# Kernel tuning notes

Hardware: AMD Instinct MI355X
Metric: run time of the kernel (lower is better)

Reference implementation:

```python
import jax, jax.numpy as jnp
import numpy as np


def setup_inputs() -> dict:
    key = jax.random.key(0)
    x = jax.random.normal(key, (32, 4096, 128), dtype=jnp.float32)
    return {"x": x, "window_size": 5}


def reference(x, window_size):
    # Circular pad along dim=1 by (w-1) using the leading slice, as in the torch code.
    w = window_size
    dim = 1
    if w > 1:
        pad = jax.lax.slice_in_dim(x, 0, w - 1, axis=dim)
        xp = jnp.concatenate([x, pad], axis=dim)  # [B, L+w-1, C]
    else:
        xp = x
    L = x.shape[dim]
    # Sliding windows of size w along dim=1: stack w shifted views -> [B, L, C, w]
    windows = jnp.stack(
        [jax.lax.slice_in_dim(xp, i, i + L, axis=dim) for i in range(w)], axis=-1
    )
    # torch.median returns the lower median: sorted[(w-1)//2]
    med = jnp.sort(windows, axis=-1)[..., (w - 1) // 2]  # [B, L, C]
    return med
```

## Files before the change

kernel.cpp:

```cpp
#include <hip/hip_runtime.h>


constexpr int B   = 32;
constexpr int L   = 4096;
constexpr int C   = 128;
constexpr int C4  = C / 4;
constexpr int RPT = 4;
constexpr int LG  = L / RPT;

typedef float f32x4 __attribute__((ext_vector_type(4)));

__device__ __forceinline__ f32x4 f4min(f32x4 a, f32x4 b) {
    f32x4 r;
    r.x = fminf(a.x, b.x); r.y = fminf(a.y, b.y);
    r.z = fminf(a.z, b.z); r.w = fminf(a.w, b.w);
    return r;
}
__device__ __forceinline__ f32x4 f4max(f32x4 a, f32x4 b) {
    f32x4 r;
    r.x = fmaxf(a.x, b.x); r.y = fmaxf(a.y, b.y);
    r.z = fmaxf(a.z, b.z); r.w = fmaxf(a.w, b.w);
    return r;
}

#define SORT2(x, y) { f32x4 _lo = f4min(x, y); f32x4 _hi = f4max(x, y); (x) = _lo; (y) = _hi; }

__device__ __forceinline__ f32x4 median5(f32x4 v0, f32x4 v1, f32x4 v2,
                                         f32x4 v3, f32x4 v4) {
    SORT2(v0, v1);
    SORT2(v3, v4);
    SORT2(v2, v4);
    SORT2(v2, v3);
    SORT2(v1, v4);
    SORT2(v0, v3);
    SORT2(v0, v2);
    SORT2(v1, v3);
    SORT2(v1, v2);
    return v2;
}

__global__ __launch_bounds__(256)
void MedianPool_73426760893099_kernel(const f32x4* __restrict__ x,
                                      f32x4* __restrict__ out) {
    const int idx = blockIdx.x * blockDim.x + threadIdx.x;
    const int c4 = idx & (C4 - 1);
    const int lg = (idx >> 5) & (LG - 1);
    const int b  = idx >> 15;

    const f32x4* __restrict__ xb = x + (size_t)b * L * C4;
    const int l0 = lg * RPT;

    f32x4 r0 = xb[(size_t)((l0 + 0) & (L - 1)) * C4 + c4];
    f32x4 r1 = xb[(size_t)((l0 + 1) & (L - 1)) * C4 + c4];
    f32x4 r2 = xb[(size_t)((l0 + 2) & (L - 1)) * C4 + c4];
    f32x4 r3 = xb[(size_t)((l0 + 3) & (L - 1)) * C4 + c4];
    f32x4 r4 = xb[(size_t)((l0 + 4) & (L - 1)) * C4 + c4];
    f32x4 r5 = xb[(size_t)((l0 + 5) & (L - 1)) * C4 + c4];
    f32x4 r6 = xb[(size_t)((l0 + 6) & (L - 1)) * C4 + c4];
    f32x4 r7 = xb[(size_t)((l0 + 7) & (L - 1)) * C4 + c4];

    f32x4 m0 = median5(r0, r1, r2, r3, r4);
    f32x4 m1 = median5(r1, r2, r3, r4, r5);
    f32x4 m2 = median5(r2, r3, r4, r5, r6);
    f32x4 m3 = median5(r3, r4, r5, r6, r7);

    f32x4* o = out + (size_t)b * L * C4 + (size_t)l0 * C4 + c4;
    __builtin_nontemporal_store(m0, o + 0 * C4);
    __builtin_nontemporal_store(m1, o + 1 * C4);
    __builtin_nontemporal_store(m2, o + 2 * C4);
    __builtin_nontemporal_store(m3, o + 3 * C4);
}

extern "C" void kernel_launch(void* const* d_in, const int* in_sizes, int n_in,
                              void* d_out, int out_size, void* d_ws, size_t ws_size,
                              hipStream_t stream) {
    const f32x4* x   = (const f32x4*)d_in[0];
    f32x4*       out = (f32x4*)d_out;

    const int threads = B * LG * C4;
    const int block   = 256;
    const int grid    = threads / block;
    MedianPool_73426760893099_kernel<<<grid, block, 0, stream>>>(x, out);
}
```

Measured before the change: 26.11 us.

## Use med3 median-of-5 network, 8 rows per thread, and XCD block swizzle

Replaces the 9-compare-exchange median-of-5 network with a shorter min/max sequence that ends in the hardware fmed3 instruction. Each thread now produces 8 output rows instead of 4, so the halo overhead drops from 8 loads per 4 outputs to 12 loads per 8 outputs. Block IDs are remapped so that contiguous work lands on the same XCD, which is meant to improve L2 reuse of the overlapping halo rows. The cost is more registers per thread and half as many threads in flight.

```diff
diff --git a/kernel.cpp b/kernel.cpp
--- a/kernel.cpp
+++ b/kernel.cpp
@@ -5,8 +5,9 @@
 constexpr int L   = 4096;
 constexpr int C   = 128;
 constexpr int C4  = C / 4;
-constexpr int RPT = 4;
+constexpr int RPT = 8;
 constexpr int LG  = L / RPT;
+constexpr int NXCD = 8;
 
 typedef float f32x4 __attribute__((ext_vector_type(4)));
 
@@ -22,53 +23,51 @@
     r.z = fmaxf(a.z, b.z); r.w = fmaxf(a.w, b.w);
     return r;
 }
+__device__ __forceinline__ f32x4 f4med3(f32x4 a, f32x4 b, f32x4 c) {
+    f32x4 r;
+    r.x = __builtin_amdgcn_fmed3f(a.x, b.x, c.x);
+    r.y = __builtin_amdgcn_fmed3f(a.y, b.y, c.y);
+    r.z = __builtin_amdgcn_fmed3f(a.z, b.z, c.z);
+    r.w = __builtin_amdgcn_fmed3f(a.w, b.w, c.w);
+    return r;
+}
 
-#define SORT2(x, y) { f32x4 _lo = f4min(x, y); f32x4 _hi = f4max(x, y); (x) = _lo; (y) = _hi; }
-
-__device__ __forceinline__ f32x4 median5(f32x4 v0, f32x4 v1, f32x4 v2,
-                                         f32x4 v3, f32x4 v4) {
-    SORT2(v0, v1);
-    SORT2(v3, v4);
-    SORT2(v2, v4);
-    SORT2(v2, v3);
-    SORT2(v1, v4);
-    SORT2(v0, v3);
-    SORT2(v0, v2);
-    SORT2(v1, v3);
-    SORT2(v1, v2);
-    return v2;
+__device__ __forceinline__ f32x4 median5(f32x4 a, f32x4 b, f32x4 c,
+                                         f32x4 d, f32x4 e) {
+    f32x4 t1 = f4min(a, b), t2 = f4max(a, b);
+    f32x4 t3 = f4min(c, d), t4 = f4max(c, d);
+    f32x4 t5 = f4max(t1, t3);
+    f32x4 t6 = f4min(t2, t4);
+    return f4med3(t5, t6, e);
 }
 
 __global__ __launch_bounds__(256)
 void MedianPool_73426760893099_kernel(const f32x4* __restrict__ x,
                                       f32x4* __restrict__ out) {
-    const int idx = blockIdx.x * blockDim.x + threadIdx.x;
+    const int nwg  = gridDim.x;
+    const int cpx  = nwg / NXCD;
+    const int bid  = (int)blockIdx.x;
+    const int bsw  = (bid % NXCD) * cpx + bid / NXCD;
+
+    const int idx = bsw * blockDim.x + threadIdx.x;
     const int c4 = idx & (C4 - 1);
     const int lg = (idx >> 5) & (LG - 1);
-    const int b  = idx >> 15;
+    const int b  = idx >> 14;
 
     const f32x4* __restrict__ xb = x + (size_t)b * L * C4;
     const int l0 = lg * RPT;
 
-    f32x4 r0 = xb[(size_t)((l0 + 0) & (L - 1)) * C4 + c4];
-    f32x4 r1 = xb[(size_t)((l0 + 1) & (L - 1)) * C4 + c4];
-    f32x4 r2 = xb[(size_t)((l0 + 2) & (L - 1)) * C4 + c4];
-    f32x4 r3 = xb[(size_t)((l0 + 3) & (L - 1)) * C4 + c4];
-    f32x4 r4 = xb[(size_t)((l0 + 4) & (L - 1)) * C4 + c4];
-    f32x4 r5 = xb[(size_t)((l0 + 5) & (L - 1)) * C4 + c4];
-    f32x4 r6 = xb[(size_t)((l0 + 6) & (L - 1)) * C4 + c4];
-    f32x4 r7 = xb[(size_t)((l0 + 7) & (L - 1)) * C4 + c4];
-
-    f32x4 m0 = median5(r0, r1, r2, r3, r4);
-    f32x4 m1 = median5(r1, r2, r3, r4, r5);
-    f32x4 m2 = median5(r2, r3, r4, r5, r6);
-    f32x4 m3 = median5(r3, r4, r5, r6, r7);
+    f32x4 r[RPT + 4];
+#pragma unroll
+    for (int i = 0; i < RPT + 4; ++i)
+        r[i] = xb[(size_t)((l0 + i) & (L - 1)) * C4 + c4];
 
     f32x4* o = out + (size_t)b * L * C4 + (size_t)l0 * C4 + c4;
-    __builtin_nontemporal_store(m0, o + 0 * C4);
-    __builtin_nontemporal_store(m1, o + 1 * C4);
-    __builtin_nontemporal_store(m2, o + 2 * C4);
-    __builtin_nontemporal_store(m3, o + 3 * C4);
+#pragma unroll
+    for (int i = 0; i < RPT; ++i) {
+        f32x4 m = median5(r[i], r[i + 1], r[i + 2], r[i + 3], r[i + 4]);
+        __builtin_nontemporal_store(m, o + i * C4);
+    }
 }
 
 extern "C" void kernel_launch(void* const* d_in, const int* in_sizes, int n_in,
```

Result: faster. 24.01 us (-8.0%).
